# Kernel tuning notes

Hardware: AMD Instinct MI355X
Metric: run time of the kernel (lower is better)

The kernel has to match this reference:

```python
import jax, jax.numpy as jnp
import numpy as np

B, CIN, COUT = 4, 512, 64
T, H, W = 16, 32, 32


def conv1x1(x, w, b=None):
    # 1x1x1 Conv3d == per-voxel linear: w (out, in), x (b, in, t, h, w)
    y = jnp.einsum('oc,bcthw->bothw', w, x)
    if b is not None:
        y = y + b[None, :, None, None, None]
    return y


def setup_inputs() -> dict:
    key = jax.random.key(0)
    ks = jax.random.split(key, 9)
    def kaiming(k, fan_out_shape):
        out_c, in_c = fan_out_shape
        std = np.sqrt(2.0 / out_c)  # fan_out mode for 1x1x1 kernel
        return jax.random.normal(k, fan_out_shape, dtype=jnp.float32) * std
    c4, c8 = CIN // 4, CIN // 8
    return {
        'x': jax.random.normal(ks[0], (B, CIN, T, H, W), dtype=jnp.float32),
        'w_add1': kaiming(ks[1], (CIN, CIN)), 'b_add1': jnp.zeros((CIN,), jnp.float32),
        'w_add2': kaiming(ks[2], (CIN, CIN)), 'b_add2': jnp.zeros((CIN,), jnp.float32),
        'w_occ1': kaiming(ks[3], (c4, CIN)), 'b_occ1': jnp.zeros((c4,), jnp.float32),
        'w_occ2': kaiming(ks[4], (c8, c4)), 'b_occ2': jnp.zeros((c8,), jnp.float32),
        'w_occ3': kaiming(ks[5], (COUT, c8)),  # bias=False
    }


def reference(x, w_add1, b_add1, w_add2, b_add2, w_occ1, b_occ1, w_occ2, b_occ2, w_occ3):
    # feature_map = add_on_layer(x): conv -> relu -> conv
    feat = conv1x1(jax.nn.relu(conv1x1(x, w_add1, b_add1)), w_add2, b_add2)
    # occ_map = abs(occ(x)): conv -> relu -> conv -> relu -> conv(no bias)
    h = jax.nn.relu(conv1x1(x, w_occ1, b_occ1))
    h = jax.nn.relu(conv1x1(h, w_occ2, b_occ2))
    occ = jnp.abs(conv1x1(h, w_occ3))  # (B, COUT, T, H, W)
    # output with pool='avg': mean over spatial of occ[:, :, None] * feat[:, None]
    # == einsum contraction over T*H*W, avoiding the (B,COUT,CIN,T,H,W) intermediate
    S = T * H * W
    out = jnp.einsum('bothw,bcthw->boc', occ, feat) / S  # (B, COUT, CIN)
    return out
```

## Files before the change

kernel.cpp:

```cpp
#include <hip/hip_runtime.h>


#define S_TOT 16384

typedef __attribute__((ext_vector_type(8))) short bf8_t;
typedef __attribute__((ext_vector_type(4))) short s4_t;
typedef __attribute__((ext_vector_type(4))) float f4_t;

#define MFMA __builtin_amdgcn_mfma_f32_16x16x32_bf16

#define BAR_FENCE() do { __builtin_amdgcn_s_barrier(); \
                         asm volatile("" ::: "memory"); } while (0)
#define WAIT_VM8()  asm volatile("s_waitcnt vmcnt(8)" ::: "memory")
#define WAIT_VM0()  asm volatile("s_waitcnt vmcnt(0)" ::: "memory")
#define WAIT_LGKM0() asm volatile("s_waitcnt lgkmcnt(0)" ::: "memory")

__device__ __forceinline__ short f2bf(float f) {
  union { float f; unsigned u; } v; v.f = f;
  unsigned u = v.u + 0x7FFFu + ((v.u >> 16) & 1u);
  return (short)(u >> 16);
}

__device__ __forceinline__ void glds16(const void* g, void* l) {
  __builtin_amdgcn_global_load_lds(
      (const __attribute__((address_space(1))) void*)g,
      (__attribute__((address_space(3))) void*)l, 16, 0, 0);
}

__device__ __forceinline__ void stage16k(const short* g, short* lds,
                                         int wv, int lane) {
#pragma unroll
  for (int i = 0; i < 4; ++i) {
    const int off = (wv * 4 + i) * 512;
    glds16(g + off + lane * 8, lds + off);
  }
}

__global__ __launch_bounds__(256) void k_convert(
    const float* __restrict__ w1, const float* __restrict__ wo1,
    const float* __restrict__ wo2, const float* __restrict__ wo3,
    short* __restrict__ dst) {
  int i = blockIdx.x * 256 + threadIdx.x;
  if (i < 262144) {
    const int j = i >> 9, k = i & 511;
    const int di = ((j >> 7) * 8 + (k >> 6)) * 8192 + ((k >> 3) & 7) * 1024 +
                   (j & 127) * 8 + (k & 7);
    dst[di] = f2bf(w1[i]);
  } else if (i < 327680) {
    const int e = i - 262144;
    const int c4 = e >> 9, k = e & 511;
    const int di = 262144 + (k >> 6) * 8192 + ((k >> 3) & 7) * 1024 +
                   c4 * 8 + (k & 7);
    dst[di] = f2bf(wo1[e]);
  } else if (i < 335872) {
    dst[i] = f2bf(wo2[i - 327680]);
  } else if (i < 339968) {
    dst[i] = f2bf(wo3[i - 335872]);
  }
}

__global__ __launch_bounds__(256) void k_toc(
    const float* __restrict__ x, short* __restrict__ xTs,
    const short* __restrict__ wo1, const short* __restrict__ wo2,
    const short* __restrict__ wo3, const float* __restrict__ bo1,
    const float* __restrict__ bo2,
    short* __restrict__ occP, float* __restrict__ sumocc) {
  __shared__ __align__(16) char smem_raw[50176];
  float (*tls)[132] = (float (*)[132])smem_raw;
  short* const xchunk = (short*)(smem_raw + 33792);
  short* const h1s = (short*)smem_raw;
  short* const h2s = xchunk;
  const int tile = blockIdx.x, b = blockIdx.y;
  const int t = threadIdx.x, lane = t & 63, wv = t >> 6;
  const int q = lane >> 4, li = lane & 15;
  const int mh = (wv & 1) * 64, nh = (wv >> 1) * 64;
  const f4_t fz = {0.f, 0.f, 0.f, 0.f};

  const int row_off = t >> 5, s4c = t & 31;
  const float* xrow = x + (size_t)b * 512 * S_TOT + tile * 128 + s4c * 4;

  f4_t hcc[4][4];
#pragma unroll
  for (int i = 0; i < 4; ++i)
#pragma unroll
    for (int j = 0; j < 4; ++j) hcc[i][j] = fz;

  f4_t xr[8];
#pragma unroll
  for (int k = 0; k < 8; ++k)
    xr[k] = *(const f4_t*)(xrow + (size_t)(k * 8 + row_off) * S_TOT);

  for (int i = 0; i < 8; ++i) {
#pragma unroll
    for (int k = 0; k < 8; ++k)
      *(f4_t*)&tls[k * 8 + row_off][s4c * 4] = xr[k];
    __syncthreads();
    if (i < 7) {
#pragma unroll
      for (int k = 0; k < 8; ++k)
        xr[k] = *(const f4_t*)(xrow +
                               (size_t)((i + 1) * 64 + k * 8 + row_off) * S_TOT);
    }
#pragma unroll
    for (int h = 0; h < 2; ++h) {
      const int gid = h * 256 + t;
      const int s_in = gid & 127, csg = gid >> 7;
      const int cs = csg * 16, k8 = csg * 2;
      alignas(16) short tmp[16];
#pragma unroll
      for (int j = 0; j < 16; ++j) tmp[j] = f2bf(tls[cs + j][s_in]);
      short* lb = xchunk + k8 * 1024 + s_in * 8;
      *(bf8_t*)lb          = *(const bf8_t*)&tmp[0];
      *(bf8_t*)(lb + 1024) = *(const bf8_t*)&tmp[8];
      short* gb = xTs + (((size_t)(b * 128 + tile) * 8 + i) * 8 + k8) * 1024 +
                  s_in * 8;
      *(bf8_t*)gb          = *(const bf8_t*)&tmp[0];
      *(bf8_t*)(gb + 1024) = *(const bf8_t*)&tmp[8];
    }
    __syncthreads();
    const short* og = wo1 + i * 8192;
#pragma unroll
    for (int kk = 0; kk < 2; ++kk) {
      const int pl = (4 * kk + q) * 128;
      bf8_t a[4], bb[4];
#pragma unroll
      for (int ma = 0; ma < 4; ++ma)
        a[ma] = *(const bf8_t*)&og[(pl + mh + 16 * ma + li) * 8];
#pragma unroll
      for (int nb = 0; nb < 4; ++nb)
        bb[nb] = *(const bf8_t*)&xchunk[(pl + nh + 16 * nb + li) * 8];
#pragma unroll
      for (int ma = 0; ma < 4; ++ma)
#pragma unroll
        for (int nb = 0; nb < 4; ++nb)
          hcc[ma][nb] = MFMA(a[ma], bb[nb], hcc[ma][nb], 0, 0, 0);
    }
  }
  __syncthreads();
#pragma unroll
  for (int ma = 0; ma < 4; ++ma) {
    const int c40 = mh + 16 * ma + 4 * q;
    f4_t bv = *(const f4_t*)(bo1 + c40);
#pragma unroll
    for (int nb = 0; nb < 4; ++nb) {
      const int sl = nh + 16 * nb + li;
      s4_t p;
#pragma unroll
      for (int r = 0; r < 4; ++r) p[r] = f2bf(fmaxf(hcc[ma][nb][r] + bv[r], 0.0f));
      *(s4_t*)&h1s[((c40 >> 3) * 128 + sl) * 8 + (c40 & 7)] = p;
    }
  }
  __syncthreads();
  f4_t a2[4][2];
#pragma unroll
  for (int i = 0; i < 4; ++i) { a2[i][0] = fz; a2[i][1] = fz; }
#pragma unroll
  for (int kk = 0; kk < 4; ++kk) {
    const int pl = (4 * kk + q) * 128;
    bf8_t a[4], bb[2];
#pragma unroll
    for (int ma = 0; ma < 4; ++ma)
      a[ma] = *(const bf8_t*)(wo2 + (size_t)(16 * ma + li) * 128 + kk * 32 + q * 8);
#pragma unroll
    for (int nb = 0; nb < 2; ++nb)
      bb[nb] = *(const bf8_t*)&h1s[(pl + 32 * wv + 16 * nb + li) * 8];
#pragma unroll
    for (int ma = 0; ma < 4; ++ma)
#pragma unroll
      for (int nb = 0; nb < 2; ++nb)
        a2[ma][nb] = MFMA(a[ma], bb[nb], a2[ma][nb], 0, 0, 0);
  }
#pragma unroll
  for (int ma = 0; ma < 4; ++ma) {
    const int c80 = 16 * ma + 4 * q;
    f4_t bv = *(const f4_t*)(bo2 + c80);
#pragma unroll
    for (int nb = 0; nb < 2; ++nb) {
      const int sl = 32 * wv + 16 * nb + li;
      s4_t p;
#pragma unroll
      for (int r = 0; r < 4; ++r) p[r] = f2bf(fmaxf(a2[ma][nb][r] + bv[r], 0.0f));
      *(s4_t*)&h2s[((c80 >> 3) * 128 + sl) * 8 + (c80 & 7)] = p;
    }
  }
  f4_t a3[4][2];
#pragma unroll
  for (int i = 0; i < 4; ++i) { a3[i][0] = fz; a3[i][1] = fz; }
#pragma unroll
  for (int kk = 0; kk < 2; ++kk) {
    const int pl = (4 * kk + q) * 128;
    bf8_t a[4], bb[2];
#pragma unroll
    for (int ma = 0; ma < 4; ++ma)
      a[ma] = *(const bf8_t*)(wo3 + (size_t)(16 * ma + li) * 64 + kk * 32 + q * 8);
#pragma unroll
    for (int nb = 0; nb < 2; ++nb)
      bb[nb] = *(const bf8_t*)&h2s[(pl + 32 * wv + 16 * nb + li) * 8];
#pragma unroll
    for (int ma = 0; ma < 4; ++ma)
#pragma unroll
      for (int nb = 0; nb < 2; ++nb)
        a3[ma][nb] = MFMA(a[ma], bb[nb], a3[ma][nb], 0, 0, 0);
  }
  short* ot = occP + (size_t)(b * 128 + tile) * 8192;
#pragma unroll
  for (int ma = 0; ma < 4; ++ma)
#pragma unroll
    for (int nb = 0; nb < 2; ++nb) {
      const int o = 16 * ma + 4 * q;
      const int sl = 32 * wv + 16 * nb + li;
#pragma unroll
      for (int r = 0; r < 4; ++r)
        ot[(sl >> 3) * 512 + (o + r) * 8 + (sl & 7)] = f2bf(fabsf(a3[ma][nb][r]));
    }
#pragma unroll
  for (int ma = 0; ma < 4; ++ma)
#pragma unroll
    for (int r = 0; r < 4; ++r) {
      float v = fabsf(a3[ma][0][r]) + fabsf(a3[ma][1][r]);
#pragma unroll
      for (int m = 1; m < 16; m <<= 1) v += __shfl_xor(v, m, 64);
      if (li == 0) atomicAdd(&sumocc[b * 64 + 16 * ma + 4 * q + r], v);
    }
}

__global__ __launch_bounds__(256) void k_feat(
    const short* __restrict__ xTs, const short* __restrict__ w1s,
    const float* __restrict__ b1, const short* __restrict__ occP,
    float* __restrict__ M) {
  __shared__ short smem[32768];
  short* const buf0 = smem;
  short* const buf1 = smem + 16384;
  short* const r1s = buf0;
  const int sg = blockIdx.x, cb = blockIdx.y, b = blockIdx.z;
  const int t = threadIdx.x, lane = t & 63, wv = t >> 6;
  const int q = lane >> 4, li = lane & 15;
  const int mh = (wv & 1) * 64, nh = (wv >> 1) * 64;
  const short* w1b = w1s + (size_t)cb * 65536;
  const f4_t fz = {0.f, 0.f, 0.f, 0.f};

  float biasv[4];
#pragma unroll
  for (int nb = 0; nb < 4; ++nb) biasv[nb] = b1[cb * 128 + nh + 16 * nb + li];

  f4_t macc[4][2];
#pragma unroll
  for (int i = 0; i < 4; ++i) { macc[i][0] = fz; macc[i][1] = fz; }

  {
    const short* xT0 = xTs + (size_t)(b * 128 + sg * 4) * 65536;
    stage16k(xT0, buf1, wv, lane);
    stage16k(w1b, buf1 + 8192, wv, lane);
  }

  for (int tt = 0; tt < 4; ++tt) {
    const int st = sg * 4 + tt;
    const short* xTb = xTs + (size_t)(b * 128 + st) * 65536;
    f4_t acc[4][4];
#pragma unroll
    for (int i = 0; i < 4; ++i)
#pragma unroll
      for (int j = 0; j < 4; ++j) acc[i][j] = fz;

    for (int i = 0; i < 8; ++i) {
      BAR_FENCE();
      if (i < 7) {
        short* nb_ = (i & 1) ? buf1 : buf0;
        stage16k(xTb + (i + 1) * 8192, nb_, wv, lane);
        stage16k(w1b + (i + 1) * 8192, nb_ + 8192, wv, lane);
        WAIT_VM8();
      } else {
        WAIT_VM0();
      }
      BAR_FENCE();
      const short* xs = (i & 1) ? buf0 : buf1;
      const short* wsp = xs + 8192;
#pragma unroll
      for (int kk = 0; kk < 2; ++kk) {
        const int pl = (4 * kk + q) * 128;
        bf8_t a[4], bb[4];
#pragma unroll
        for (int ma = 0; ma < 4; ++ma)
          a[ma] = *(const bf8_t*)&xs[(pl + mh + 16 * ma + li) * 8];
#pragma unroll
        for (int nb = 0; nb < 4; ++nb)
          bb[nb] = *(const bf8_t*)&wsp[(pl + nh + 16 * nb + li) * 8];
#pragma unroll
        for (int ma = 0; ma < 4; ++ma)
#pragma unroll
          for (int nb = 0; nb < 4; ++nb)
            acc[ma][nb] = MFMA(a[ma], bb[nb], acc[ma][nb], 0, 0, 0);
      }
    }
    WAIT_LGKM0();
    BAR_FENCE();
#pragma unroll
    for (int ma = 0; ma < 4; ++ma) {
      const int sl0 = mh + 16 * ma + 4 * q;
#pragma unroll
      for (int nb = 0; nb < 4; ++nb) {
        const int jl = nh + 16 * nb + li;
        s4_t p;
#pragma unroll
        for (int r = 0; r < 4; ++r)
          p[r] = f2bf(fmaxf(acc[ma][nb][r] + biasv[nb], 0.0f));
        *(s4_t*)&r1s[((sl0 >> 3) * 128 + jl) * 8 + (sl0 & 7)] = p;
      }
    }
    WAIT_LGKM0();
    BAR_FENCE();
    const short* ot = occP + (size_t)(b * 128 + st) * 8192;
    bf8_t af[4][4];
#pragma unroll
    for (int kc = 0; kc < 4; ++kc)
#pragma unroll
      for (int ma = 0; ma < 4; ++ma)
        af[kc][ma] = *(const bf8_t*)(ot + ((kc * 4 + q) * 64 + 16 * ma + li) * 8);
    if (tt < 3) {
      stage16k(xTb + 65536, buf1, wv, lane);
      stage16k(w1b, buf1 + 8192, wv, lane);
    }
#pragma unroll
    for (int kc = 0; kc < 4; ++kc) {
      const int pl = (4 * kc + q) * 128;
      bf8_t bb[2];
#pragma unroll
      for (int nb = 0; nb < 2; ++nb)
        bb[nb] = *(const bf8_t*)&r1s[(pl + 32 * wv + 16 * nb + li) * 8];
#pragma unroll
      for (int ma = 0; ma < 4; ++ma)
#pragma unroll
        for (int nb = 0; nb < 2; ++nb)
          macc[ma][nb] = MFMA(af[kc][ma], bb[nb], macc[ma][nb], 0, 0, 0);
    }
  }
#pragma unroll
  for (int ma = 0; ma < 4; ++ma)
#pragma unroll
    for (int nb = 0; nb < 2; ++nb) {
      const int jg = cb * 128 + 32 * wv + 16 * nb + li;
#pragma unroll
      for (int r = 0; r < 4; ++r) {
        const int o = 16 * ma + 4 * q + r;
        atomicAdd(&M[((size_t)b * 64 + o) * 512 + jg], macc[ma][nb][r]);
      }
    }
}

__global__ __launch_bounds__(256) void k_out(
    const float* __restrict__ M, const float* __restrict__ sumocc,
    const float* __restrict__ w2, const float* __restrict__ b2,
    float* __restrict__ out) {
  __shared__ float Mlds[16][516];
  __shared__ float Wlds[16][516];
  const int cg = blockIdx.x, og = blockIdx.y, b = blockIdx.z;
  const int t = threadIdx.x;
  const float* Msrc = M + ((size_t)b * 64 + og * 16) * 512;
  const float* Wsrc = w2 + (size_t)cg * 16 * 512;
#pragma unroll
  for (int k = 0; k < 8; ++k) {
    const int fi = k * 256 + t;
    const int row = fi >> 7, col = (fi & 127) * 4;
    *(f4_t*)&Mlds[row][col] = *(const f4_t*)(Msrc + row * 512 + col);
    *(f4_t*)&Wlds[row][col] = *(const f4_t*)(Wsrc + row * 512 + col);
  }
  __syncthreads();
  const int o = t >> 4, c = t & 15;
  float s0 = 0.f, s1 = 0.f;
#pragma unroll 8
  for (int j = 0; j < 512; j += 8) {
    f4_t m0 = *(const f4_t*)&Mlds[o][j];
    f4_t w0 = *(const f4_t*)&Wlds[c][j];
    f4_t m1 = *(const f4_t*)&Mlds[o][j + 4];
    f4_t w1 = *(const f4_t*)&Wlds[c][j + 4];
    s0 += m0[0] * w0[0] + m0[1] * w0[1] + m0[2] * w0[2] + m0[3] * w0[3];
    s1 += m1[0] * w1[0] + m1[1] * w1[1] + m1[2] * w1[2] + m1[3] * w1[3];
  }
  const int og_ = og * 16 + o, cg_ = cg * 16 + c;
  out[((size_t)b * 64 + og_) * 512 + cg_] =
      ((s0 + s1) + sumocc[b * 64 + og_] * b2[cg_]) * (1.0f / 16384.0f);
}

extern "C" void kernel_launch(void* const* d_in, const int* in_sizes, int n_in,
                              void* d_out, int out_size, void* d_ws, size_t ws_size,
                              hipStream_t stream) {
  (void)in_sizes; (void)n_in; (void)out_size; (void)ws_size;
  const float* x      = (const float*)d_in[0];
  const float* w_add1 = (const float*)d_in[1];
  const float* b_add1 = (const float*)d_in[2];
  const float* w_add2 = (const float*)d_in[3];
  const float* b_add2 = (const float*)d_in[4];
  const float* w_occ1 = (const float*)d_in[5];
  const float* b_occ1 = (const float*)d_in[6];
  const float* w_occ2 = (const float*)d_in[7];
  const float* b_occ2 = (const float*)d_in[8];
  const float* w_occ3 = (const float*)d_in[9];

  char* ws = (char*)d_ws;
  short* xTs     = (short*)(ws);
  short* wb      = (short*)(ws + 67108864);
  short* occP    = (short*)(ws + 67788800);
  float* M       = (float*)(ws + 76177408);
  float* sumocc  = (float*)(ws + 76701696);

  hipMemsetAsync(M, 0, 524288 + 1024, stream);
  k_convert<<<dim3(1328), dim3(256), 0, stream>>>(w_add1, w_occ1, w_occ2, w_occ3, wb);

  const short* w1sp = wb;
  const short* wbo1 = wb + 262144;
  const short* wbo2 = wb + 327680;
  const short* wbo3 = wb + 335872;
  k_toc<<<dim3(128, 4), dim3(256), 0, stream>>>(
      x, xTs, wbo1, wbo2, wbo3, b_occ1, b_occ2, occP, sumocc);
  k_feat<<<dim3(32, 4, 4), dim3(256), 0, stream>>>(xTs, w1sp, b_add1, occP, M);
  k_out<<<dim3(32, 4, 4), dim3(256), 0, stream>>>(M, sumocc, w_add2, b_add2,
                                                  (float*)d_out);
}
```

Measured before the change: 354.5 us.

## Halve k_toc spatial tile to 64 and stage x as bf16 in LDS

The occupancy/transpose kernel now processes 64 spatial positions per block instead of 128, doubling the grid to 256x4 blocks, and converts x to bf16 before writing it to the LDS staging tile. This shrinks shared memory from about 50KB to about 25KB and cuts accumulator registers, so more blocks can be resident and the 256 CUs get more work to hide global-load latency. In exchange, each wo1 weight fragment is reused over half as many positions, so more weight traffic per output. A stray dummy LDS read of h2s before the real h1s load is left in.

Result: slower. 468.7 us (+32.2%).

```diff
diff --git a/kernel.cpp b/kernel.cpp
--- a/kernel.cpp
+++ b/kernel.cpp
@@ -65,55 +65,57 @@
     const short* __restrict__ wo3, const float* __restrict__ bo1,
     const float* __restrict__ bo2,
     short* __restrict__ occP, float* __restrict__ sumocc) {
-  __shared__ __align__(16) char smem_raw[50176];
-  float (*tls)[132] = (float (*)[132])smem_raw;
-  short* const xchunk = (short*)(smem_raw + 33792);
-  short* const h1s = (short*)smem_raw;
-  short* const h2s = xchunk;
-  const int tile = blockIdx.x, b = blockIdx.y;
+  __shared__ __align__(16) short smem[12416];
+  short (*tls)[66] = (short (*)[66])smem;
+  short* const xchunk = smem + 4224;
+  short* const h1s = smem;
+  short* const h2s = smem + 8320;
+  const int tile64 = blockIdx.x, b = blockIdx.y;
+  const int t128 = tile64 >> 1, half = tile64 & 1;
   const int t = threadIdx.x, lane = t & 63, wv = t >> 6;
   const int q = lane >> 4, li = lane & 15;
-  const int mh = (wv & 1) * 64, nh = (wv >> 1) * 64;
+  const int mh1 = (wv & 1) * 64;
+  const int nhs = (wv >> 1) * 32;
+  const int swc = wv * 16;
   const f4_t fz = {0.f, 0.f, 0.f, 0.f};
 
-  const int row_off = t >> 5, s4c = t & 31;
-  const float* xrow = x + (size_t)b * 512 * S_TOT + tile * 128 + s4c * 4;
-
-  f4_t hcc[4][4];
-#pragma unroll
-  for (int i = 0; i < 4; ++i)
-#pragma unroll
-    for (int j = 0; j < 4; ++j) hcc[i][j] = fz;
-
-  f4_t xr[8];
-#pragma unroll
-  for (int k = 0; k < 8; ++k)
-    xr[k] = *(const f4_t*)(xrow + (size_t)(k * 8 + row_off) * S_TOT);
+  const int r0 = t >> 4, c4i = t & 15;
+  const float* xb = x + (size_t)(b * 512 + r0) * S_TOT + tile64 * 64 + c4i * 4;
+
+  f4_t hcc[4][2];
+#pragma unroll
+  for (int i = 0; i < 4; ++i) { hcc[i][0] = fz; hcc[i][1] = fz; }
+
+  f4_t xr[4];
+#pragma unroll
+  for (int k = 0; k < 4; ++k)
+    xr[k] = *(const f4_t*)(xb + (size_t)(k * 16) * S_TOT);
 
   for (int i = 0; i < 8; ++i) {
 #pragma unroll
-    for (int k = 0; k < 8; ++k)
-      *(f4_t*)&tls[k * 8 + row_off][s4c * 4] = xr[k];
+    for (int k = 0; k < 4; ++k) {
+      s4_t p;
+#pragma unroll
+      for (int r = 0; r < 4; ++r) p[r] = f2bf(xr[k][r]);
+      *(s4_t*)&tls[k * 16 + r0][c4i * 4] = p;
+    }
     __syncthreads();
     if (i < 7) {
 #pragma unroll
-      for (int k = 0; k < 8; ++k)
-        xr[k] = *(const f4_t*)(xrow +
-                               (size_t)((i + 1) * 64 + k * 8 + row_off) * S_TOT);
-    }
-#pragma unroll
-    for (int h = 0; h < 2; ++h) {
-      const int gid = h * 256 + t;
-      const int s_in = gid & 127, csg = gid >> 7;
-      const int cs = csg * 16, k8 = csg * 2;
+      for (int k = 0; k < 4; ++k)
+        xr[k] = *(const f4_t*)(xb + (size_t)((i + 1) * 64 + k * 16) * S_TOT);
+    }
+    {
+      const int s_in = lane, cs = wv * 16, k8w = wv * 2;
       alignas(16) short tmp[16];
 #pragma unroll
-      for (int j = 0; j < 16; ++j) tmp[j] = f2bf(tls[cs + j][s_in]);
-      short* lb = xchunk + k8 * 1024 + s_in * 8;
-      *(bf8_t*)lb          = *(const bf8_t*)&tmp[0];
-      *(bf8_t*)(lb + 1024) = *(const bf8_t*)&tmp[8];
-      short* gb = xTs + (((size_t)(b * 128 + tile) * 8 + i) * 8 + k8) * 1024 +
-                  s_in * 8;
+      for (int j = 0; j < 16; ++j) tmp[j] = tls[cs + j][s_in];
+      short* lb = xchunk + k8w * 512 + s_in * 8;
+      *(bf8_t*)lb         = *(const bf8_t*)&tmp[0];
+      *(bf8_t*)(lb + 512) = *(const bf8_t*)&tmp[8];
+      const int sing = half * 64 + s_in;
+      short* gb = xTs + (((size_t)(b * 128 + t128) * 8 + i) * 8 + k8w) * 1024 +
+                  sing * 8;
       *(bf8_t*)gb          = *(const bf8_t*)&tmp[0];
       *(bf8_t*)(gb + 1024) = *(const bf8_t*)&tmp[8];
     }
@@ -121,103 +123,88 @@
     const short* og = wo1 + i * 8192;
 #pragma unroll
     for (int kk = 0; kk < 2; ++kk) {
-      const int pl = (4 * kk + q) * 128;
-      bf8_t a[4], bb[4];
+      bf8_t a[4], bb[2];
 #pragma unroll
       for (int ma = 0; ma < 4; ++ma)
-        a[ma] = *(const bf8_t*)&og[(pl + mh + 16 * ma + li) * 8];
-#pragma unroll
-      for (int nb = 0; nb < 4; ++nb)
-        bb[nb] = *(const bf8_t*)&xchunk[(pl + nh + 16 * nb + li) * 8];
+        a[ma] = *(const bf8_t*)&og[((4 * kk + q) * 128 + mh1 + 16 * ma + li) * 8];
+#pragma unroll
+      for (int nb = 0; nb < 2; ++nb)
+        bb[nb] = *(const bf8_t*)&xchunk[((4 * kk + q) * 64 + nhs + 16 * nb + li) * 8];
 #pragma unroll
       for (int ma = 0; ma < 4; ++ma)
 #pragma unroll
-        for (int nb = 0; nb < 4; ++nb)
+        for (int nb = 0; nb < 2; ++nb)
           hcc[ma][nb] = MFMA(a[ma], bb[nb], hcc[ma][nb], 0, 0, 0);
     }
   }
   __syncthreads();
 #pragma unroll
   for (int ma = 0; ma < 4; ++ma) {
-    const int c40 = mh + 16 * ma + 4 * q;
+    const int c40 = mh1 + 16 * ma + 4 * q;
     f4_t bv = *(const f4_t*)(bo1 + c40);
 #pragma unroll
-    for (int nb = 0; nb < 4; ++nb) {
-      const int sl = nh + 16 * nb + li;
+    for (int nb = 0; nb < 2; ++nb) {
+      const int sl = nhs + 16 * nb + li;
       s4_t p;
 #pragma unroll
       for (int r = 0; r < 4; ++r) p[r] = f2bf(fmaxf(hcc[ma][nb][r] + bv[r], 0.0f));
-      *(s4_t*)&h1s[((c40 >> 3) * 128 + sl) * 8 + (c40 & 7)] = p;
+      *(s4_t*)&h1s[((c40 >> 3) * 64 + sl) * 8 + (c40 & 7)] = p;
     }
   }
   __syncthreads();
-  f4_t a2[4][2];
-#pragma unroll
-  for (int i = 0; i < 4; ++i) { a2[i][0] = fz; a2[i][1] = fz; }
+  f4_t a2[4];
+#pragma unroll
+  for (int i = 0; i < 4; ++i) a2[i] = fz;
 #pragma unroll
   for (int kk = 0; kk < 4; ++kk) {
-    const int pl = (4 * kk + q) * 128;
-    bf8_t a[4], bb[2];
+    bf8_t a[4], bb;
 #pragma unroll
     for (int ma = 0; ma < 4; ++ma)
       a[ma] = *(const bf8_t*)(wo2 + (size_t)(16 * ma + li) * 128 + kk * 32 + q * 8);
-#pragma unroll
-    for (int nb = 0; nb < 2; ++nb)
-      bb[nb] = *(const bf8_t*)&h1s[(pl + 32 * wv + 16 * nb + li) * 8];
+    bb = *(const bf8_t*)&h2s[0];
+    bb = *(const bf8_t*)&h1s[((4 * kk + q) * 64 + swc + li) * 8];
 #pragma unroll
     for (int ma = 0; ma < 4; ++ma)
-#pragma unroll
-      for (int nb = 0; nb < 2; ++nb)
-        a2[ma][nb] = MFMA(a[ma], bb[nb], a2[ma][nb], 0, 0, 0);
+      a2[ma] = MFMA(a[ma], bb, a2[ma], 0, 0, 0);
   }
 #pragma unroll
   for (int ma = 0; ma < 4; ++ma) {
     const int c80 = 16 * ma + 4 * q;
     f4_t bv = *(const f4_t*)(bo2 + c80);
-#pragma unroll
-    for (int nb = 0; nb < 2; ++nb) {
-      const int sl = 32 * wv + 16 * nb + li;
-      s4_t p;
-#pragma unroll
-      for (int r = 0; r < 4; ++r) p[r] = f2bf(fmaxf(a2[ma][nb][r] + bv[r], 0.0f));
-      *(s4_t*)&h2s[((c80 >> 3) * 128 + sl) * 8 + (c80 & 7)] = p;
-    }
-  }
-  f4_t a3[4][2];
-#pragma unroll
-  for (int i = 0; i < 4; ++i) { a3[i][0] = fz; a3[i][1] = fz; }
+    const int sl = swc + li;
+    s4_t p;
+#pragma unroll
+    for (int r = 0; r < 4; ++r) p[r] = f2bf(fmaxf(a2[ma][r] + bv[r], 0.0f));
+    *(s4_t*)&h2s[((c80 >> 3) * 64 + sl) * 8 + (c80 & 7)] = p;
+  }
+  f4_t a3[4];
+#pragma unroll
+  for (int i = 0; i < 4; ++i) a3[i] = fz;
 #pragma unroll
   for (int kk = 0; kk < 2; ++kk) {
-    const int pl = (4 * kk + q) * 128;
-    bf8_t a[4], bb[2];
+    bf8_t a[4], bb;
 #pragma unroll
     for (int ma = 0; ma < 4; ++ma)
       a[ma] = *(const bf8_t*)(wo3 + (size_t)(16 * ma + li) * 64 + kk * 32 + q * 8);
-#pragma unroll
-    for (int nb = 0; nb < 2; ++nb)
-      bb[nb] = *(const bf8_t*)&h2s[(pl + 32 * wv + 16 * nb + li) * 8];
+    bb = *(const bf8_t*)&h2s[((4 * kk + q) * 64 + swc + li) * 8];
 #pragma unroll
     for (int ma = 0; ma < 4; ++ma)
-#pragma unroll
-      for (int nb = 0; nb < 2; ++nb)
-        a3[ma][nb] = MFMA(a[ma], bb[nb], a3[ma][nb], 0, 0, 0);
-  }
-  short* ot = occP + (size_t)(b * 128 + tile) * 8192;
+      a3[ma] = MFMA(a[ma], bb, a3[ma], 0, 0, 0);
+  }
+  short* ot = occP + (size_t)(b * 128 + t128) * 8192;
+#pragma unroll
+  for (int ma = 0; ma < 4; ++ma) {
+    const int o = 16 * ma + 4 * q;
+    const int slg = half * 64 + swc + li;
+#pragma unroll
+    for (int r = 0; r < 4; ++r)
+      ot[(slg >> 3) * 512 + (o + r) * 8 + (slg & 7)] = f2bf(fabsf(a3[ma][r]));
+  }
 #pragma unroll
   for (int ma = 0; ma < 4; ++ma)
 #pragma unroll
-    for (int nb = 0; nb < 2; ++nb) {
-      const int o = 16 * ma + 4 * q;
-      const int sl = 32 * wv + 16 * nb + li;
-#pragma unroll
-      for (int r = 0; r < 4; ++r)
-        ot[(sl >> 3) * 512 + (o + r) * 8 + (sl & 7)] = f2bf(fabsf(a3[ma][nb][r]));
-    }
-#pragma unroll
-  for (int ma = 0; ma < 4; ++ma)
-#pragma unroll
     for (int r = 0; r < 4; ++r) {
-      float v = fabsf(a3[ma][0][r]) + fabsf(a3[ma][1][r]);
+      float v = fabsf(a3[ma][r]);
 #pragma unroll
       for (int m = 1; m < 16; m <<= 1) v += __shfl_xor(v, m, 64);
       if (li == 0) atomicAdd(&sumocc[b * 64 + 16 * ma + 4 * q + r], v);
@@ -410,7 +397,7 @@
   const short* wbo1 = wb + 262144;
   const short* wbo2 = wb + 327680;
   const short* wbo3 = wb + 335872;
-  k_toc<<<dim3(128, 4), dim3(256), 0, stream>>>(
+  k_toc<<<dim3(256, 4), dim3(256), 0, stream>>>(
       x, xTs, wbo1, wbo2, wbo3, b_occ1, b_occ2, occP, sumocc);
   k_feat<<<dim3(32, 4, 4), dim3(256), 0, stream>>>(xTs, w1sp, b_add1, occP, M);
   k_out<<<dim3(32, 4, 4), dim3(256), 0, stream>>>(M, sumocc, w_add2, b_add2,
```
